# Kernel optimization log

Hardware: AMD Instinct MI355X
Metric: run time of the kernel (lower is better)

## Reference

```python
import jax, jax.numpy as jnp
import numpy as np

N = 100000
F_IN = 128
HID = 256
NUM_CLASSES = 64
E = 1600000


def setup_inputs() -> dict:
    key = jax.random.key(0)
    ks = jax.random.split(key, 10)
    x = jax.random.normal(ks[0], (N, F_IN), dtype=jnp.float32)
    edge_index = jax.random.randint(ks[1], (2, E), 0, N, dtype=jnp.int32)
    edge_weight = jax.random.uniform(ks[2], (E,), dtype=jnp.float32)
    def glorot(k, shape):
        lim = np.sqrt(6.0 / (shape[0] + shape[1]))
        return jax.random.uniform(k, shape, jnp.float32, -lim, lim)
    W0 = glorot(ks[3], (F_IN, HID)); b0 = jnp.zeros((HID,), jnp.float32)
    W1 = glorot(ks[4], (HID, HID)); b1 = jnp.zeros((HID,), jnp.float32)
    W2 = glorot(ks[5], (HID, NUM_CLASSES)); b2 = jnp.zeros((NUM_CLASSES,), jnp.float32)
    return {"x": x, "edge_index": edge_index, "edge_weight": edge_weight,
            "W0": W0, "b0": b0, "W1": W1, "b1": b1, "W2": W2, "b2": b2}


def _gcn_norm(edge_index, edge_weight, n_nodes):
    # renormalization trick: add self-loops (weight 1), D^-1/2 A D^-1/2
    loop = jnp.arange(n_nodes, dtype=edge_index.dtype)
    src = jnp.concatenate([edge_index[0], loop])
    dst = jnp.concatenate([edge_index[1], loop])
    w = jnp.concatenate([edge_weight, jnp.ones((n_nodes,), edge_weight.dtype)])
    deg = jax.ops.segment_sum(w, dst, num_segments=n_nodes)
    d_inv_sqrt = jnp.where(deg > 0, jax.lax.rsqrt(jnp.maximum(deg, 1e-12)), 0.0)
    norm = d_inv_sqrt[src] * w * d_inv_sqrt[dst]
    return src, dst, norm


def _gcn_layer(x, src, dst, norm, W, b, act):
    h = x @ W                                  # [N, d_out] project first (cheap dense)
    msg = h[src] * norm[:, None]               # [E+N, d_out] gather + scale
    out = jax.ops.segment_sum(msg, dst, num_segments=x.shape[0]) + b
    return act(out) if act is not None else out


def reference(x, edge_index, edge_weight, W0, b0, W1, b1, W2, b2):
    n_nodes = x.shape[0]
    src, dst, norm = _gcn_norm(edge_index, edge_weight, n_nodes)
    # dropout is identity at inference (training=None)
    h = _gcn_layer(x, src, dst, norm, W0, b0, jax.nn.relu)
    h = _gcn_layer(h, src, dst, norm, W1, b1, jax.nn.relu)
    h = _gcn_layer(h, src, dst, norm, W2, b2, None)
    return h
```

## Files before the change

kernel.cpp:

```cpp
#include <hip/hip_runtime.h>

#define N_NODES 100000
#define F_IN 128
#define HID 256
#define NCLS 64
#define N_EDGES 1600000

typedef _Float16 f16;
typedef f16 half8 __attribute__((ext_vector_type(8)));
typedef f16 half4 __attribute__((ext_vector_type(4)));
typedef float f32x4 __attribute__((ext_vector_type(4)));
typedef unsigned long long u64;
typedef unsigned short u16;

#define FIXED_SCALE 67108864.0f

__global__ void k_init(unsigned long long* __restrict__ degp, int n) {
    int i = blockIdx.x * 256 + threadIdx.x;
    if (i < n) degp[i] = (unsigned long long)(1u << 26);
}

#define EB4  1563
#define XB   12500
#define W0B  128
#define W1B  256
#define W2B  64
__global__ __launch_bounds__(256) void mega1(
        const int* __restrict__ dst, const float* __restrict__ ew,
        unsigned long long* __restrict__ degp, u16* __restrict__ seq,
        const float* __restrict__ x, f16* __restrict__ xh,
        const float* __restrict__ W0, f16* __restrict__ Wt0,
        const float* __restrict__ W1, f16* __restrict__ Wt1,
        const float* __restrict__ W2, f16* __restrict__ Wt2) {
    int bid = blockIdx.x;
    int t = threadIdx.x;
    if (bid < EB4) {
        int base = bid * 1024 + t;
        int d[4]; unsigned long long c[4]; unsigned long long old[4];
        bool ok[4];
        #pragma unroll
        for (int j = 0; j < 4; ++j) {
            int i = base + j * 256;
            ok[j] = (i < N_EDGES);
            if (ok[j]) {
                d[j] = dst[i];
                c[j] = (1ULL << 40) |
                    (unsigned long long)__float2uint_rn(ew[i] * FIXED_SCALE);
            }
        }
        #pragma unroll
        for (int j = 0; j < 4; ++j)
            if (ok[j]) old[j] = atomicAdd(&degp[d[j]], c[j]);
        #pragma unroll
        for (int j = 0; j < 4; ++j)
            if (ok[j]) seq[base + j * 256] = (u16)(old[j] >> 40);
    } else if (bid < EB4 + XB) {
        int i = (bid - EB4) * 256 + t;
        if (i < N_NODES * (F_IN / 4)) {
            float4 v = *(const float4*)&x[(size_t)i * 4];
            half4 o;
            o[0] = (f16)v.x; o[1] = (f16)v.y; o[2] = (f16)v.z; o[3] = (f16)v.w;
            *(half4*)&xh[(size_t)i * 4] = o;
        }
    } else if (bid < EB4 + XB + W0B) {
        int i = (bid - EB4 - XB) * 256 + t;
        int k = i / HID, dd = i % HID;
        Wt0[dd * F_IN + k] = (f16)W0[i];
    } else if (bid < EB4 + XB + W0B + W1B) {
        int i = (bid - EB4 - XB - W0B) * 256 + t;
        int k = i / HID, dd = i % HID;
        Wt1[dd * HID + k] = (f16)W1[i];
    } else {
        int i = (bid - EB4 - XB - W0B - W1B) * 256 + t;
        int k = i / NCLS, dd = i % NCLS;
        Wt2[dd * HID + k] = (f16)W2[i];
    }
}

__global__ void k_scan1(const unsigned long long* __restrict__ degp,
                        int* __restrict__ cnt, float* __restrict__ dis,
                        float* __restrict__ selfnorm,
                        int* __restrict__ incl, int* __restrict__ bsum, int n) {
    __shared__ int s[256];
    int t = threadIdx.x;
    int i = blockIdx.x * 256 + t;
    int v = 0;
    if (i < n) {
        unsigned long long p = degp[i];
        v = (int)(p >> 40);
        cnt[i] = v;
        float deg = (float)(p & ((1ULL << 40) - 1)) * (1.0f / FIXED_SCALE);
        float d = rsqrtf(deg);
        dis[i] = d;
        selfnorm[i] = d * d;
    }
    s[t] = v;
    __syncthreads();
    #pragma unroll
    for (int off = 1; off < 256; off <<= 1) {
        int x = (t >= off) ? s[t - off] : 0;
        __syncthreads();
        s[t] += x;
        __syncthreads();
    }
    if (i < n) incl[i] = s[t];
    if (t == 255) bsum[blockIdx.x] = s[255];
}

__global__ void k_scan2(const int* __restrict__ bsum, int* __restrict__ boff, int nb) {
    __shared__ int s[512];
    int t = threadIdx.x;
    int v = (t < nb) ? bsum[t] : 0;
    s[t] = v;
    __syncthreads();
    #pragma unroll
    for (int off = 1; off < 512; off <<= 1) {
        int x = (t >= off) ? s[t - off] : 0;
        __syncthreads();
        s[t] += x;
        __syncthreads();
    }
    if (t < nb) boff[t] = s[t] - v;
}

__global__ void k_place(const int* __restrict__ src, const int* __restrict__ dst,
                        const float* __restrict__ w, const u16* __restrict__ seq,
                        const int* __restrict__ incl, const int* __restrict__ cnt,
                        const int* __restrict__ boff, const float* __restrict__ dis,
                        int2* __restrict__ csr, int e) {
    int i = blockIdx.x * 256 + threadIdx.x;
    if (i < e) {
        int s = src[i], d = dst[i];
        float nw = dis[s] * w[i] * dis[d];
        int pos = incl[d] - cnt[d] + boff[d >> 8] + (int)seq[i];
        csr[pos] = make_int2(s, __float_as_int(nw));
    }
}

template <int K, int DOUT, bool BIAS_RELU>
__global__ __launch_bounds__(256) void gemm_mfma(const f16* __restrict__ in,
                                                 const f16* __restrict__ Wt,
                                                 const float* __restrict__ bias,
                                                 f16* __restrict__ out,
                                                 int nNodes) {
    constexpr int BM = 128, BN = 64, BK = 32;
    constexpr int NB = DOUT / BN;
    constexpr int AP = 40;
    constexpr int CP = 72;
    constexpr int SMEM = (BM * AP + BN * AP) > (BM * CP) ? (BM * AP + BN * AP) : (BM * CP);
    __shared__ f16 smem[SMEM];
    f16* As = smem;
    f16* Bs = smem + BM * AP;

    const int nwg = gridDim.x;
    const int b = blockIdx.x;
    const int q = nwg >> 3, r = nwg & 7, xcd = b & 7;
    const int wk = (xcd < r ? xcd * (q + 1) : r * (q + 1) + (xcd - r) * q) + (b >> 3);
    const int bx = wk / NB, by = wk % NB;

    const int t = threadIdx.x;
    const int w = t >> 6;
    const int lane = t & 63;
    const int quad = lane >> 4;
    const int l16 = lane & 15;
    const int nodeBase = bx * BM;
    const int colBase = by * BN;

    f32x4 acc[2][4] = {};

    for (int k0 = 0; k0 < K; k0 += BK) {
        {
            int koff = (t & 3) * 8;
            #pragma unroll
            for (int p = 0; p < 2; ++p) {
                int r2 = (t >> 2) + p * 64;
                int gn = nodeBase + r2;
                if (gn >= nNodes) gn = nNodes - 1;
                half8 v = *(const half8*)&in[(size_t)gn * K + k0 + koff];
                *(half8*)&As[r2 * AP + koff] = v;
            }
        }
        {
            int koff = (t & 3) * 8;
            int c = t >> 2;
            half8 v = *(const half8*)&Wt[(size_t)(colBase + c) * K + k0 + koff];
            *(half8*)&Bs[c * AP + koff] = v;
        }
        __syncthreads();

        half8 a[2];
        #pragma unroll
        for (int rt = 0; rt < 2; ++rt)
            a[rt] = *(const half8*)&As[(w * 32 + rt * 16 + l16) * AP + quad * 8];
        #pragma unroll
        for (int ct = 0; ct < 4; ++ct) {
            half8 bf = *(const half8*)&Bs[(ct * 16 + l16) * AP + quad * 8];
            acc[0][ct] = __builtin_amdgcn_mfma_f32_16x16x32_f16(a[0], bf, acc[0][ct], 0, 0, 0);
            acc[1][ct] = __builtin_amdgcn_mfma_f32_16x16x32_f16(a[1], bf, acc[1][ct], 0, 0, 0);
        }
        __syncthreads();
    }

    float bv[4];
    #pragma unroll
    for (int ct = 0; ct < 4; ++ct)
        bv[ct] = BIAS_RELU ? bias[colBase + ct * 16 + l16] : 0.0f;

    f16* Cs = smem;
    #pragma unroll
    for (int rt = 0; rt < 2; ++rt)
        #pragma unroll
        for (int ct = 0; ct < 4; ++ct)
            #pragma unroll
            for (int rr2 = 0; rr2 < 4; ++rr2) {
                int rr = w * 32 + rt * 16 + quad * 4 + rr2;
                int cc = ct * 16 + l16;
                float v = acc[rt][ct][rr2];
                if (BIAS_RELU) v = fmaxf(v + bv[ct], 0.0f);
                Cs[rr * CP + cc] = (f16)v;
            }
    __syncthreads();
    #pragma unroll
    for (int p = 0; p < 4; ++p) {
        int rr = (t >> 3) + p * 32;
        int gn = nodeBase + rr;
        int chunk = (t & 7) * 8;
        if (gn < nNodes)
            *(half8*)&out[(size_t)gn * DOUT + colBase + chunk] =
                *(const half8*)&Cs[rr * CP + chunk];
    }
}

template <int DOUT, int TPN, bool HAS_BIAS, bool OUT_F32>
__global__ __launch_bounds__(256) void agg_csr(const f16* __restrict__ h,
                                               const int2* __restrict__ csr,
                                               const int* __restrict__ incl,
                                               const int* __restrict__ cnt,
                                               const int* __restrict__ boff,
                                               const float* __restrict__ sn,
                                               const float* __restrict__ bias,
                                               void* __restrict__ outv,
                                               int nodeBase, int nodeEnd) {
    constexpr int NPB = 256 / TPN;
    int node = nodeBase + blockIdx.x * NPB + threadIdx.x / TPN;
    if (node >= nodeEnd) return;
    int lane = threadIdx.x % TPN;
    int col = lane * 8;

    float s = sn[node];
    half8 hv = *(const half8*)&h[(size_t)node * DOUT + col];
    float acc[8];
    #pragma unroll
    for (int i = 0; i < 8; ++i)
        acc[i] = s * (float)hv[i] + (HAS_BIAS ? bias[col + i] : 0.0f);

    int c = cnt[node];
    int end = incl[node] + boff[node >> 8];
    int e = end - c;

    for (; e + 1 < end; e += 2) {
        int2 e0 = csr[e], e1 = csr[e + 1];
        float w0 = __int_as_float(e0.y), w1 = __int_as_float(e1.y);
        half8 a0 = *(const half8*)&h[(size_t)e0.x * DOUT + col];
        half8 a1 = *(const half8*)&h[(size_t)e1.x * DOUT + col];
        #pragma unroll
        for (int i = 0; i < 8; ++i) acc[i] += w0 * (float)a0[i] + w1 * (float)a1[i];
    }
    if (e < end) {
        int2 e0 = csr[e];
        float w0 = __int_as_float(e0.y);
        half8 a0 = *(const half8*)&h[(size_t)e0.x * DOUT + col];
        #pragma unroll
        for (int i = 0; i < 8; ++i) acc[i] += w0 * (float)a0[i];
    }

    if (OUT_F32) {
        float* out = (float*)outv;
        float4 r0 = make_float4(acc[0], acc[1], acc[2], acc[3]);
        float4 r1 = make_float4(acc[4], acc[5], acc[6], acc[7]);
        *(float4*)&out[(size_t)node * DOUT + col] = r0;
        *(float4*)&out[(size_t)node * DOUT + col + 4] = r1;
    } else {
        f16* out = (f16*)outv;
        half8 o;
        #pragma unroll
        for (int i = 0; i < 8; ++i) o[i] = (f16)acc[i];
        *(half8*)&out[(size_t)node * DOUT + col] = o;
    }
}

extern "C" void kernel_launch(void* const* d_in, const int* in_sizes, int n_in,
                              void* d_out, int out_size, void* d_ws, size_t ws_size,
                              hipStream_t stream) {
    const float* x  = (const float*)d_in[0];
    const int*   ei = (const int*)d_in[1];
    const float* ew = (const float*)d_in[2];
    const float* W0 = (const float*)d_in[3];
    const float* b0 = (const float*)d_in[4];
    const float* W1 = (const float*)d_in[5];
    const float* b1 = (const float*)d_in[6];
    const float* W2 = (const float*)d_in[7];
    const float* b2 = (const float*)d_in[8];
    const int* src = ei;
    const int* dst = ei + N_EDGES;
    float* outp = (float*)d_out;

    char* ws = (char*)d_ws;
    unsigned long long* degp = (unsigned long long*)ws;  ws += N_NODES * 8;
    int2*  csr      = (int2*)ws;   ws += (size_t)N_EDGES * 8;
    u16*   seq      = (u16*)ws;    ws += (size_t)N_EDGES * 4;
    float* dis      = (float*)ws;  ws += N_NODES * 4;
    float* selfnorm = (float*)ws;  ws += N_NODES * 4;
    int*   cnt      = (int*)ws;    ws += N_NODES * 4;
    int*   incl     = (int*)ws;    ws += N_NODES * 4;
    int*   bsum     = (int*)ws;    ws += 512 * 4;
    int*   boff     = (int*)ws;    ws += 512 * 4;
    f16*   xh       = (f16*)ws;    ws += (size_t)N_NODES * F_IN * 2;
    f16*   Wt0      = (f16*)ws;    ws += F_IN * HID * 2;
    f16*   Wt1      = (f16*)ws;    ws += HID * HID * 2;
    f16*   Wt2      = (f16*)ws;    ws += HID * NCLS * 2;
    f16*   bufA     = (f16*)ws;    ws += (size_t)N_NODES * HID * 2;
    f16*   bufB     = (f16*)ws;    ws += (size_t)N_NODES * HID * 2;

    const int nb = (N_NODES + 255) / 256;
    const int eb = (N_EDGES + 255) / 256;

    k_init<<<nb, 256, 0, stream>>>(degp, N_NODES);
    mega1<<<EB4 + XB + W0B + W1B + W2B, 256, 0, stream>>>(
        dst, ew, degp, seq, x, xh, W0, Wt0, W1, Wt1, W2, Wt2);
    k_scan1<<<nb, 256, 0, stream>>>(degp, cnt, dis, selfnorm, incl, bsum, N_NODES);
    k_scan2<<<1, 512, 0, stream>>>(bsum, boff, nb);
    k_place<<<eb, 256, 0, stream>>>(src, dst, ew, seq, incl, cnt, boff, dis, csr, N_EDGES);

    const int gX = (N_NODES + 127) / 128;
    const int HALF = N_NODES / 2;

    agg_csr<F_IN, 16, false, false><<<(N_NODES + 15) / 16, 256, 0, stream>>>(
        xh, csr, incl, cnt, boff, selfnorm, nullptr, bufA, 0, N_NODES);
    gemm_mfma<F_IN, HID, true><<<gX * (HID / 64), 256, 0, stream>>>(bufA, Wt0, b0, bufB, N_NODES);

    agg_csr<HID, 32, false, false><<<HALF / 8, 256, 0, stream>>>(
        bufB, csr, incl, cnt, boff, selfnorm, nullptr, bufA, 0, HALF);
    agg_csr<HID, 32, false, false><<<(N_NODES - HALF + 7) / 8, 256, 0, stream>>>(
        bufB, csr, incl, cnt, boff, selfnorm, nullptr, bufA, HALF, N_NODES);
    gemm_mfma<HID, HID, true><<<gX * (HID / 64), 256, 0, stream>>>(bufA, Wt1, b1, bufB, N_NODES);

    gemm_mfma<HID, NCLS, false><<<gX * (NCLS / 64), 256, 0, stream>>>(bufB, Wt2, nullptr, bufA, N_NODES);
    agg_csr<NCLS, 8, true, true><<<(N_NODES + 31) / 32, 256, 0, stream>>>(
        bufA, csr, incl, cnt, boff, selfnorm, b2, outp, 0, N_NODES);
}
```

Before: 541.3 us.

## Shard degree counters into eight slices and compute degrees from CSR

```diff
diff --git a/kernel.cpp b/kernel.cpp
--- a/kernel.cpp
+++ b/kernel.cpp
@@ -12,12 +12,11 @@
 typedef float f32x4 __attribute__((ext_vector_type(4)));
 typedef unsigned long long u64;
 typedef unsigned short u16;
-
-#define FIXED_SCALE 67108864.0f
-
-__global__ void k_init(unsigned long long* __restrict__ degp, int n) {
+typedef unsigned int u32;
+
+__global__ void k_init(u32* __restrict__ cnt8, int n8) {
     int i = blockIdx.x * 256 + threadIdx.x;
-    if (i < n) degp[i] = (unsigned long long)(1u << 26);
+    if (i < n8) cnt8[i] = 0u;
 }
 
 #define EB4  1563
@@ -26,8 +25,8 @@
 #define W1B  256
 #define W2B  64
 __global__ __launch_bounds__(256) void mega1(
-        const int* __restrict__ dst, const float* __restrict__ ew,
-        unsigned long long* __restrict__ degp, u16* __restrict__ seq,
+        const int* __restrict__ dst,
+        u32* __restrict__ cnt8, u16* __restrict__ seq,
         const float* __restrict__ x, f16* __restrict__ xh,
         const float* __restrict__ W0, f16* __restrict__ Wt0,
         const float* __restrict__ W1, f16* __restrict__ Wt1,
@@ -35,25 +34,22 @@
     int bid = blockIdx.x;
     int t = threadIdx.x;
     if (bid < EB4) {
+        const int j = bid & 7;
+        u32* myc = cnt8 + (size_t)j * N_NODES;
         int base = bid * 1024 + t;
-        int d[4]; unsigned long long c[4]; unsigned long long old[4];
-        bool ok[4];
-        #pragma unroll
-        for (int j = 0; j < 4; ++j) {
-            int i = base + j * 256;
-            ok[j] = (i < N_EDGES);
-            if (ok[j]) {
-                d[j] = dst[i];
-                c[j] = (1ULL << 40) |
-                    (unsigned long long)__float2uint_rn(ew[i] * FIXED_SCALE);
-            }
-        }
-        #pragma unroll
-        for (int j = 0; j < 4; ++j)
-            if (ok[j]) old[j] = atomicAdd(&degp[d[j]], c[j]);
-        #pragma unroll
-        for (int j = 0; j < 4; ++j)
-            if (ok[j]) seq[base + j * 256] = (u16)(old[j] >> 40);
+        int d[4]; u32 old[4]; bool ok[4];
+        #pragma unroll
+        for (int u = 0; u < 4; ++u) {
+            int i = base + u * 256;
+            ok[u] = (i < N_EDGES);
+            if (ok[u]) d[u] = dst[i];
+        }
+        #pragma unroll
+        for (int u = 0; u < 4; ++u)
+            if (ok[u]) old[u] = atomicAdd(&myc[d[u]], 1u);
+        #pragma unroll
+        for (int u = 0; u < 4; ++u)
+            if (ok[u]) seq[base + u * 256] = (u16)((j << 12) | old[u]);
     } else if (bid < EB4 + XB) {
         int i = (bid - EB4) * 256 + t;
         if (i < N_NODES * (F_IN / 4)) {
@@ -77,22 +73,30 @@
     }
 }
 
-__global__ void k_scan1(const unsigned long long* __restrict__ degp,
-                        int* __restrict__ cnt, float* __restrict__ dis,
-                        float* __restrict__ selfnorm,
+__global__ void k_scan1(const u32* __restrict__ cnt8,
+                        int* __restrict__ cnt, u16* __restrict__ sliceoff,
                         int* __restrict__ incl, int* __restrict__ bsum, int n) {
     __shared__ int s[256];
     int t = threadIdx.x;
     int i = blockIdx.x * 256 + t;
     int v = 0;
     if (i < n) {
-        unsigned long long p = degp[i];
-        v = (int)(p >> 40);
+        u32 off = 0;
+        u16 so[8];
+        #pragma unroll
+        for (int j = 0; j < 8; ++j) {
+            u32 c = cnt8[(size_t)j * N_NODES + i];
+            so[j] = (u16)off;
+            off += c;
+        }
+        v = (int)off;
         cnt[i] = v;
-        float deg = (float)(p & ((1ULL << 40) - 1)) * (1.0f / FIXED_SCALE);
-        float d = rsqrtf(deg);
-        dis[i] = d;
-        selfnorm[i] = d * d;
+        uint4 p;
+        p.x = (u32)so[0] | ((u32)so[1] << 16);
+        p.y = (u32)so[2] | ((u32)so[3] << 16);
+        p.z = (u32)so[4] | ((u32)so[5] << 16);
+        p.w = (u32)so[6] | ((u32)so[7] << 16);
+        *(uint4*)&sliceoff[(size_t)i * 8] = p;
     }
     s[t] = v;
     __syncthreads();
@@ -126,14 +130,49 @@
 __global__ void k_place(const int* __restrict__ src, const int* __restrict__ dst,
                         const float* __restrict__ w, const u16* __restrict__ seq,
                         const int* __restrict__ incl, const int* __restrict__ cnt,
-                        const int* __restrict__ boff, const float* __restrict__ dis,
+                        const int* __restrict__ boff, const u16* __restrict__ sliceoff,
                         int2* __restrict__ csr, int e) {
     int i = blockIdx.x * 256 + threadIdx.x;
     if (i < e) {
         int s = src[i], d = dst[i];
-        float nw = dis[s] * w[i] * dis[d];
-        int pos = incl[d] - cnt[d] + boff[d >> 8] + (int)seq[i];
-        csr[pos] = make_int2(s, __float_as_int(nw));
+        u16 sq = seq[i];
+        int j = sq >> 12, slot = sq & 0xFFF;
+        int pos = incl[d] - cnt[d] + boff[d >> 8] + (int)sliceoff[(size_t)d * 8 + j] + slot;
+        csr[pos] = make_int2(s, __float_as_int(w[i]));
+    }
+}
+
+__global__ void k_deg(const int2* __restrict__ csr,
+                      const int* __restrict__ incl, const int* __restrict__ cnt,
+                      const int* __restrict__ boff,
+                      float* __restrict__ dis, float* __restrict__ selfnorm, int n) {
+    int i = blockIdx.x * 256 + threadIdx.x;
+    if (i < n) {
+        int c = cnt[i];
+        int end = incl[i] + boff[i >> 8];
+        float deg = 1.0f;
+        for (int e = end - c; e < end; ++e)
+            deg += __int_as_float(csr[e].y);
+        float d = rsqrtf(deg);
+        dis[i] = d;
+        selfnorm[i] = d * d;
+    }
+}
+
+__global__ void k_normw(int2* __restrict__ csr,
+                        const int* __restrict__ incl, const int* __restrict__ cnt,
+                        const int* __restrict__ boff,
+                        const float* __restrict__ dis, int n) {
+    int i = blockIdx.x * 256 + threadIdx.x;
+    if (i < n) {
+        int c = cnt[i];
+        int end = incl[i] + boff[i >> 8];
+        float dd = dis[i];
+        for (int e = end - c; e < end; ++e) {
+            int2 en = csr[e];
+            float nw = dis[en.x] * __int_as_float(en.y) * dd;
+            csr[e] = make_int2(en.x, __float_as_int(nw));
+        }
     }
 }
 
@@ -306,9 +345,10 @@
     float* outp = (float*)d_out;
 
     char* ws = (char*)d_ws;
-    unsigned long long* degp = (unsigned long long*)ws;  ws += N_NODES * 8;
+    u32*   cnt8     = (u32*)ws;    ws += (size_t)8 * N_NODES * 4;
     int2*  csr      = (int2*)ws;   ws += (size_t)N_EDGES * 8;
     u16*   seq      = (u16*)ws;    ws += (size_t)N_EDGES * 4;
+    u16*   sliceoff = (u16*)ws;    ws += (size_t)N_NODES * 8 * 2;
     float* dis      = (float*)ws;  ws += N_NODES * 4;
     float* selfnorm = (float*)ws;  ws += N_NODES * 4;
     int*   cnt      = (int*)ws;    ws += N_NODES * 4;
@@ -325,12 +365,14 @@
     const int nb = (N_NODES + 255) / 256;
     const int eb = (N_EDGES + 255) / 256;
 
-    k_init<<<nb, 256, 0, stream>>>(degp, N_NODES);
+    k_init<<<(8 * N_NODES + 255) / 256, 256, 0, stream>>>(cnt8, 8 * N_NODES);
     mega1<<<EB4 + XB + W0B + W1B + W2B, 256, 0, stream>>>(
-        dst, ew, degp, seq, x, xh, W0, Wt0, W1, Wt1, W2, Wt2);
-    k_scan1<<<nb, 256, 0, stream>>>(degp, cnt, dis, selfnorm, incl, bsum, N_NODES);
+        dst, cnt8, seq, x, xh, W0, Wt0, W1, Wt1, W2, Wt2);
+    k_scan1<<<nb, 256, 0, stream>>>(cnt8, cnt, sliceoff, incl, bsum, N_NODES);
     k_scan2<<<1, 512, 0, stream>>>(bsum, boff, nb);
-    k_place<<<eb, 256, 0, stream>>>(src, dst, ew, seq, incl, cnt, boff, dis, csr, N_EDGES);
+    k_place<<<eb, 256, 0, stream>>>(src, dst, ew, seq, incl, cnt, boff, sliceoff, csr, N_EDGES);
+    k_deg<<<nb, 256, 0, stream>>>(csr, incl, cnt, boff, dis, selfnorm, N_NODES);
+    k_normw<<<nb, 256, 0, stream>>>(csr, incl, cnt, boff, dis, N_NODES);
 
     const int gX = (N_NODES + 127) / 128;
     const int HALF = N_NODES / 2;
```

New measurement: 572.3 us. 5.7% more time.

## Split degree atomics across eight slices and precompute CSR row offsets

Applied to the files above, without the earlier changes.

```diff
diff --git a/kernel.cpp b/kernel.cpp
--- a/kernel.cpp
+++ b/kernel.cpp
@@ -12,12 +12,13 @@
 typedef float f32x4 __attribute__((ext_vector_type(4)));
 typedef unsigned long long u64;
 typedef unsigned short u16;
+typedef unsigned int u32;
 
 #define FIXED_SCALE 67108864.0f
 
-__global__ void k_init(unsigned long long* __restrict__ degp, int n) {
+__global__ void k_init(u64* __restrict__ degp8, int n8) {
     int i = blockIdx.x * 256 + threadIdx.x;
-    if (i < n) degp[i] = (unsigned long long)(1u << 26);
+    if (i < n8) degp8[i] = (i < N_NODES) ? (u64)(1u << 26) : 0ull;
 }
 
 #define EB4  1563
@@ -27,7 +28,7 @@
 #define W2B  64
 __global__ __launch_bounds__(256) void mega1(
         const int* __restrict__ dst, const float* __restrict__ ew,
-        unsigned long long* __restrict__ degp, u16* __restrict__ seq,
+        u64* __restrict__ degp8, u16* __restrict__ seq,
         const float* __restrict__ x, f16* __restrict__ xh,
         const float* __restrict__ W0, f16* __restrict__ Wt0,
         const float* __restrict__ W1, f16* __restrict__ Wt1,
@@ -35,25 +36,26 @@
     int bid = blockIdx.x;
     int t = threadIdx.x;
     if (bid < EB4) {
+        const int j = bid & 7;
+        u64* myp = degp8 + (size_t)j * N_NODES;
         int base = bid * 1024 + t;
-        int d[4]; unsigned long long c[4]; unsigned long long old[4];
-        bool ok[4];
-        #pragma unroll
-        for (int j = 0; j < 4; ++j) {
-            int i = base + j * 256;
-            ok[j] = (i < N_EDGES);
-            if (ok[j]) {
-                d[j] = dst[i];
-                c[j] = (1ULL << 40) |
-                    (unsigned long long)__float2uint_rn(ew[i] * FIXED_SCALE);
+        int d[4]; u64 c[4], old[4]; bool ok[4];
+        #pragma unroll
+        for (int u = 0; u < 4; ++u) {
+            int i = base + u * 256;
+            ok[u] = (i < N_EDGES);
+            if (ok[u]) {
+                d[u] = dst[i];
+                c[u] = (1ULL << 40) |
+                    (u64)__float2uint_rn(ew[i] * FIXED_SCALE);
             }
         }
         #pragma unroll
-        for (int j = 0; j < 4; ++j)
-            if (ok[j]) old[j] = atomicAdd(&degp[d[j]], c[j]);
-        #pragma unroll
-        for (int j = 0; j < 4; ++j)
-            if (ok[j]) seq[base + j * 256] = (u16)(old[j] >> 40);
+        for (int u = 0; u < 4; ++u)
+            if (ok[u]) old[u] = atomicAdd(&myp[d[u]], c[u]);
+        #pragma unroll
+        for (int u = 0; u < 4; ++u)
+            if (ok[u]) seq[base + u * 256] = (u16)((j << 12) | (u32)(old[u] >> 40));
     } else if (bid < EB4 + XB) {
         int i = (bid - EB4) * 256 + t;
         if (i < N_NODES * (F_IN / 4)) {
@@ -77,22 +79,37 @@
     }
 }
 
-__global__ void k_scan1(const unsigned long long* __restrict__ degp,
+__global__ void k_scan1(const u64* __restrict__ degp8,
                         int* __restrict__ cnt, float* __restrict__ dis,
-                        float* __restrict__ selfnorm,
+                        float* __restrict__ selfnorm, u16* __restrict__ sliceoff,
                         int* __restrict__ incl, int* __restrict__ bsum, int n) {
     __shared__ int s[256];
     int t = threadIdx.x;
     int i = blockIdx.x * 256 + t;
     int v = 0;
     if (i < n) {
-        unsigned long long p = degp[i];
-        v = (int)(p >> 40);
+        u32 off = 0;
+        u64 wsum = 0;
+        u16 so[8];
+        #pragma unroll
+        for (int j = 0; j < 8; ++j) {
+            u64 p = degp8[(size_t)j * N_NODES + i];
+            so[j] = (u16)off;
+            off += (u32)(p >> 40);
+            wsum += (p & ((1ULL << 40) - 1));
+        }
+        v = (int)off;
         cnt[i] = v;
-        float deg = (float)(p & ((1ULL << 40) - 1)) * (1.0f / FIXED_SCALE);
+        float deg = (float)wsum * (1.0f / FIXED_SCALE);
         float d = rsqrtf(deg);
         dis[i] = d;
         selfnorm[i] = d * d;
+        uint4 p4;
+        p4.x = (u32)so[0] | ((u32)so[1] << 16);
+        p4.y = (u32)so[2] | ((u32)so[3] << 16);
+        p4.z = (u32)so[4] | ((u32)so[5] << 16);
+        p4.w = (u32)so[6] | ((u32)so[7] << 16);
+        *(uint4*)&sliceoff[(size_t)i * 8] = p4;
     }
     s[t] = v;
     __syncthreads();
@@ -123,16 +140,23 @@
     if (t < nb) boff[t] = s[t] - v;
 }
 
+__global__ void k_scan3(int* __restrict__ row, const int* __restrict__ incl,
+                        const int* __restrict__ cnt, const int* __restrict__ boff, int n) {
+    int i = blockIdx.x * 256 + threadIdx.x;
+    if (i < n) row[i] = incl[i] - cnt[i] + boff[i >> 8];
+}
+
 __global__ void k_place(const int* __restrict__ src, const int* __restrict__ dst,
                         const float* __restrict__ w, const u16* __restrict__ seq,
-                        const int* __restrict__ incl, const int* __restrict__ cnt,
-                        const int* __restrict__ boff, const float* __restrict__ dis,
+                        const int* __restrict__ row, const u16* __restrict__ sliceoff,
+                        const float* __restrict__ dis,
                         int2* __restrict__ csr, int e) {
     int i = blockIdx.x * 256 + threadIdx.x;
     if (i < e) {
         int s = src[i], d = dst[i];
         float nw = dis[s] * w[i] * dis[d];
-        int pos = incl[d] - cnt[d] + boff[d >> 8] + (int)seq[i];
+        u16 sq = seq[i];
+        int pos = row[d] + (int)sliceoff[(size_t)d * 8 + (sq >> 12)] + (int)(sq & 0xFFF);
         csr[pos] = make_int2(s, __float_as_int(nw));
     }
 }
@@ -234,9 +258,8 @@
 template <int DOUT, int TPN, bool HAS_BIAS, bool OUT_F32>
 __global__ __launch_bounds__(256) void agg_csr(const f16* __restrict__ h,
                                                const int2* __restrict__ csr,
-                                               const int* __restrict__ incl,
+                                               const int* __restrict__ row,
                                                const int* __restrict__ cnt,
-                                               const int* __restrict__ boff,
                                                const float* __restrict__ sn,
                                                const float* __restrict__ bias,
                                                void* __restrict__ outv,
@@ -254,9 +277,8 @@
     for (int i = 0; i < 8; ++i)
         acc[i] = s * (float)hv[i] + (HAS_BIAS ? bias[col + i] : 0.0f);
 
-    int c = cnt[node];
-    int end = incl[node] + boff[node >> 8];
-    int e = end - c;
+    int e = row[node];
+    int end = e + cnt[node];
 
     for (; e + 1 < end; e += 2) {
         int2 e0 = csr[e], e1 = csr[e + 1];
@@ -306,13 +328,15 @@
     float* outp = (float*)d_out;
 
     char* ws = (char*)d_ws;
-    unsigned long long* degp = (unsigned long long*)ws;  ws += N_NODES * 8;
+    u64*   degp8    = (u64*)ws;    ws += (size_t)8 * N_NODES * 8;
     int2*  csr      = (int2*)ws;   ws += (size_t)N_EDGES * 8;
     u16*   seq      = (u16*)ws;    ws += (size_t)N_EDGES * 4;
+    u16*   sliceoff = (u16*)ws;    ws += (size_t)N_NODES * 8 * 2;
     float* dis      = (float*)ws;  ws += N_NODES * 4;
     float* selfnorm = (float*)ws;  ws += N_NODES * 4;
     int*   cnt      = (int*)ws;    ws += N_NODES * 4;
     int*   incl     = (int*)ws;    ws += N_NODES * 4;
+    int*   row      = (int*)ws;    ws += N_NODES * 4;
     int*   bsum     = (int*)ws;    ws += 512 * 4;
     int*   boff     = (int*)ws;    ws += 512 * 4;
     f16*   xh       = (f16*)ws;    ws += (size_t)N_NODES * F_IN * 2;
@@ -325,27 +349,28 @@
     const int nb = (N_NODES + 255) / 256;
     const int eb = (N_EDGES + 255) / 256;
 
-    k_init<<<nb, 256, 0, stream>>>(degp, N_NODES);
+    k_init<<<(8 * N_NODES + 255) / 256, 256, 0, stream>>>(degp8, 8 * N_NODES);
     mega1<<<EB4 + XB + W0B + W1B + W2B, 256, 0, stream>>>(
-        dst, ew, degp, seq, x, xh, W0, Wt0, W1, Wt1, W2, Wt2);
-    k_scan1<<<nb, 256, 0, stream>>>(degp, cnt, dis, selfnorm, incl, bsum, N_NODES);
+        dst, ew, degp8, seq, x, xh, W0, Wt0, W1, Wt1, W2, Wt2);
+    k_scan1<<<nb, 256, 0, stream>>>(degp8, cnt, dis, selfnorm, sliceoff, incl, bsum, N_NODES);
     k_scan2<<<1, 512, 0, stream>>>(bsum, boff, nb);
-    k_place<<<eb, 256, 0, stream>>>(src, dst, ew, seq, incl, cnt, boff, dis, csr, N_EDGES);
+    k_scan3<<<nb, 256, 0, stream>>>(row, incl, cnt, boff, N_NODES);
+    k_place<<<eb, 256, 0, stream>>>(src, dst, ew, seq, row, sliceoff, dis, csr, N_EDGES);
 
     const int gX = (N_NODES + 127) / 128;
     const int HALF = N_NODES / 2;
 
     agg_csr<F_IN, 16, false, false><<<(N_NODES + 15) / 16, 256, 0, stream>>>(
-        xh, csr, incl, cnt, boff, selfnorm, nullptr, bufA, 0, N_NODES);
+        xh, csr, row, cnt, selfnorm, nullptr, bufA, 0, N_NODES);
     gemm_mfma<F_IN, HID, true><<<gX * (HID / 64), 256, 0, stream>>>(bufA, Wt0, b0, bufB, N_NODES);
 
     agg_csr<HID, 32, false, false><<<HALF / 8, 256, 0, stream>>>(
-        bufB, csr, incl, cnt, boff, selfnorm, nullptr, bufA, 0, HALF);
+        bufB, csr, row, cnt, selfnorm, nullptr, bufA, 0, HALF);
     agg_csr<HID, 32, false, false><<<(N_NODES - HALF + 7) / 8, 256, 0, stream>>>(
-        bufB, csr, incl, cnt, boff, selfnorm, nullptr, bufA, HALF, N_NODES);
+        bufB, csr, row, cnt, selfnorm, nullptr, bufA, HALF, N_NODES);
     gemm_mfma<HID, HID, true><<<gX * (HID / 64), 256, 0, stream>>>(bufA, Wt1, b1, bufB, N_NODES);
 
     gemm_mfma<HID, NCLS, false><<<gX * (NCLS / 64), 256, 0, stream>>>(bufB, Wt2, nullptr, bufA, N_NODES);
     agg_csr<NCLS, 8, true, true><<<(N_NODES + 31) / 32, 256, 0, stream>>>(
-        bufA, csr, incl, cnt, boff, selfnorm, b2, outp, 0, N_NODES);
-}
+        bufA, csr, row, cnt, selfnorm, b2, outp, 0, N_NODES);
+}
```

After: 547.5 us. No clear change (+1.2%).
